# Kernel optimization log

Measured on AMD Instinct MI355X. Metric: run time of the kernel, lower is better.

## Reference

```python
import jax, jax.numpy as jnp
import numpy as np

B, L, C, D = 32, 4096, 64, 128
TOPK = max(1, int(L * 0.5))


def setup_inputs() -> dict:
    key = jax.random.key(0)
    ks = jax.random.split(key, 9)
    s = lambda k, sh: jax.random.normal(k, sh, dtype=jnp.float32) * 0.02
    return {
        "x": jax.random.normal(ks[0], (B, L, C), dtype=jnp.float32),
        "score_w": s(ks[1], (C,)),
        "score_b": jnp.zeros((), jnp.float32),
        "sparse_w": s(ks[2], (C, D)),
        "sparse_b": jnp.zeros((D,), jnp.float32),
        "full_w": s(ks[3], (C, D)),
        "full_b": jnp.zeros((D,), jnp.float32),
        "ln_g": jnp.ones((D,), jnp.float32),
        "ln_b": jnp.zeros((D,), jnp.float32),
    }


def _layernorm(h, g, b, eps=1e-5):
    mu = jnp.mean(h, axis=-1, keepdims=True)
    var = jnp.mean(jnp.square(h - mu), axis=-1, keepdims=True)
    return (h - mu) * jax.lax.rsqrt(var + eps) * g + b


def reference(x, score_w, score_b, sparse_w, sparse_b, full_w, full_b, ln_g, ln_b):
    # scores: (B, L)
    scores = jnp.einsum("blc,c->bl", x, score_w) + score_b
    _, idx = jax.lax.top_k(scores, TOPK)              # (B, K)
    sparse_x = jnp.take_along_axis(x, idx[:, :, None], axis=1)  # (B, K, C)
    sparse_feat = jax.nn.gelu(jnp.einsum("bkc,cd->bkd", sparse_x, sparse_w) + sparse_b, approximate=False)
    sparse_agg = jnp.mean(sparse_feat, axis=1, keepdims=True)   # (B, 1, D)
    full_feat = jnp.einsum("blc,cd->bld", x, full_w) + full_b   # (B, L, D)
    out = _layernorm(full_feat + sparse_agg, ln_g, ln_b)
    return out
```

## Files before the change

kernel.cpp:

```cpp
#include <hip/hip_runtime.h>
#include <math.h>

static constexpr int PB = 32;
static constexpr int PL = 4096;
static constexpr int PC = 64;
static constexpr int PD = 128;
static constexpr int PK = 2048;

typedef __attribute__((ext_vector_type(8))) short bf16x8;
typedef __attribute__((ext_vector_type(4))) float f32x4;

#define MFMA_BF16(A, B, C) __builtin_amdgcn_mfma_f32_16x16x32_bf16(A, B, C, 0, 0, 0)

__device__ inline short f2bf(float f) {
  unsigned u = __float_as_uint(f);
  u += 0x7FFFu + ((u >> 16) & 1u);
  return (short)(u >> 16);
}

__device__ inline unsigned f2key(float f) {
  unsigned u = __float_as_uint(f);
  return (u & 0x80000000u) ? ~u : (u | 0x80000000u);
}

__global__ __launch_bounds__(256) void scores_kernel(
    const float* __restrict__ x, const float* __restrict__ score_w,
    const float* __restrict__ score_b, const float* __restrict__ sparse_w,
    const float* __restrict__ full_w, float* __restrict__ scores,
    short* __restrict__ xbf, unsigned* __restrict__ wtfg,
    unsigned* __restrict__ ghist) {
  int tid = threadIdx.x;
  int blk = blockIdx.x;
  int b = blk >> 5;

  if (blk < 2) {
    const float* w = (blk == 0) ? sparse_w : full_w;
    unsigned* dst = wtfg + blk * 4096;
    for (int i = tid; i < 4096; i += 256) {
      int d = i & 127, cp = i >> 7, c = cp * 2;
      float va = w[(size_t)c * PD + d];
      float vb = w[(size_t)(c + 1) * PD + d];
      unsigned lo = (unsigned short)f2bf(va);
      unsigned hi = (unsigned short)f2bf(vb);
      int t = d >> 4, dl = d & 15, h = c >> 5, cq = (c >> 3) & 3, jp = (c & 7) >> 1;
      dst[(((t * 2 + h) * 4 + cq) * 16 + dl) * 4 + jp] = lo | (hi << 16);
    }
  }

  int r  = tid >> 4;
  int c4 = tid & 15;
  float4 wv = *(const float4*)(score_w + c4 * 4);
  float sb0 = score_b[0];
  unsigned* gh = ghist + (size_t)b * 2048;

  #pragma unroll
  for (int it = 0; it < 8; ++it) {
    int row = blk * 128 + it * 16 + r;
    float4 xv = *(const float4*)(x + (size_t)row * PC + c4 * 4);
    short4 xbv;
    xbv.x = f2bf(xv.x); xbv.y = f2bf(xv.y); xbv.z = f2bf(xv.z); xbv.w = f2bf(xv.w);
    *(short4*)(xbf + (size_t)row * PC + c4 * 4) = xbv;
    float v = xv.x * wv.x + xv.y * wv.y + xv.z * wv.z + xv.w * wv.w;
    #pragma unroll
    for (int off = 1; off < 16; off <<= 1) v += __shfl_xor(v, off);
    if (c4 == 0) {
      float sv = v + sb0;
      scores[row] = sv;
      atomicAdd(&gh[f2key(sv) >> 21], 1u);
    }
  }
}

template <int N>
__device__ inline void suffix_scan(const unsigned* cnt, int tid, int lane, int wid,
                                   unsigned* hbuf, unsigned* wsum) {
  unsigned tsum = 0;
  #pragma unroll
  for (int i = 0; i < N; ++i) tsum += cnt[i];
  unsigned v = tsum;
  #pragma unroll
  for (int off = 1; off < 64; off <<= 1) {
    unsigned t = __shfl_down(v, off);
    if (lane + off < 64) v += t;
  }
  if (lane == 0) wsum[wid] = v;
  __syncthreads();
  unsigned add = 0;
  #pragma unroll
  for (int w = 0; w < 4; ++w) if (w > wid) add += wsum[w];
  unsigned run = v + add - tsum;
  #pragma unroll
  for (int i = N - 1; i >= 0; --i) { run += cnt[i]; hbuf[tid * N + i] = run; }
  if (tid == 0) hbuf[256 * N] = 0;
  __syncthreads();
}

__global__ __launch_bounds__(256) void select_kernel(
    const float* __restrict__ scores, const unsigned* __restrict__ ghist,
    int* __restrict__ selidx, float* __restrict__ agg) {
  __shared__ unsigned hbuf[2049];
  __shared__ unsigned wsum[4];
  __shared__ unsigned sh_pfx, sh_need;

  int tid = threadIdx.x;
  int lane = tid & 63;
  int wid  = tid >> 6;
  int b = blockIdx.x;
  const float* sc = scores + (size_t)b * PL;

  unsigned k[16];
  #pragma unroll
  for (int q = 0; q < 4; ++q) {
    float4 f = *(const float4*)(sc + tid * 16 + q * 4);
    k[q * 4 + 0] = f2key(f.x);
    k[q * 4 + 1] = f2key(f.y);
    k[q * 4 + 2] = f2key(f.z);
    k[q * 4 + 3] = f2key(f.w);
  }
  if (tid == 0) sh_need = (unsigned)PK;
  if (tid < PD) agg[(size_t)b * PD + tid] = 0.f;

  {
    const unsigned* gh = ghist + (size_t)b * 2048;
    uint4 c0 = *(const uint4*)(gh + tid * 8);
    uint4 c1 = *(const uint4*)(gh + tid * 8 + 4);
    unsigned cnt[8] = {c0.x, c0.y, c0.z, c0.w, c1.x, c1.y, c1.z, c1.w};
    suffix_scan<8>(cnt, tid, lane, wid, hbuf, wsum);
    unsigned need = sh_need;
    #pragma unroll
    for (int i = 0; i < 8; ++i) {
      int kk = tid * 8 + i;
      if (hbuf[kk] >= need && hbuf[kk + 1] < need) {
        sh_pfx  = (unsigned)kk << 21;
        sh_need = need - hbuf[kk + 1];
      }
    }
  }

  {
    #pragma unroll
    for (int i = 0; i < 8; ++i) hbuf[tid * 8 + i] = 0u;
    __syncthreads();
    unsigned pfx = sh_pfx, need = sh_need;
    #pragma unroll
    for (int j = 0; j < 16; ++j) {
      if ((k[j] & 0xFFE00000u) == pfx)
        atomicAdd(&hbuf[(k[j] >> 10) & 2047u], 1u);
    }
    __syncthreads();
    unsigned cnt[8];
    #pragma unroll
    for (int i = 0; i < 8; ++i) cnt[i] = hbuf[tid * 8 + i];
    __syncthreads();
    suffix_scan<8>(cnt, tid, lane, wid, hbuf, wsum);
    #pragma unroll
    for (int i = 0; i < 8; ++i) {
      int kk = tid * 8 + i;
      if (hbuf[kk] >= need && hbuf[kk + 1] < need) {
        sh_pfx  = pfx | ((unsigned)kk << 10);
        sh_need = need - hbuf[kk + 1];
      }
    }
  }

  {
    #pragma unroll
    for (int i = 0; i < 4; ++i) hbuf[tid * 4 + i] = 0u;
    __syncthreads();
    unsigned pfx = sh_pfx, need = sh_need;
    #pragma unroll
    for (int j = 0; j < 16; ++j) {
      if ((k[j] & 0xFFFFFC00u) == pfx)
        atomicAdd(&hbuf[k[j] & 1023u], 1u);
    }
    __syncthreads();
    unsigned cnt[4];
    #pragma unroll
    for (int i = 0; i < 4; ++i) cnt[i] = hbuf[tid * 4 + i];
    __syncthreads();
    suffix_scan<4>(cnt, tid, lane, wid, hbuf, wsum);
    #pragma unroll
    for (int i = 0; i < 4; ++i) {
      int kk = tid * 4 + i;
      if (hbuf[kk] >= need && hbuf[kk + 1] < need) {
        sh_pfx  = pfx | (unsigned)kk;
        sh_need = need - hbuf[kk + 1];
      }
    }
  }
  __syncthreads();
  unsigned T = sh_pfx;
  unsigned needEq = sh_need;

  int base = tid * 16;
  unsigned ceq = 0;
  #pragma unroll
  for (int j = 0; j < 16; ++j) ceq += (k[j] == T);

  unsigned v1 = ceq;
  #pragma unroll
  for (int off = 1; off < 64; off <<= 1) {
    unsigned t = __shfl_up(v1, off);
    if (lane >= off) v1 += t;
  }
  if (lane == 63) wsum[wid] = v1;
  __syncthreads();
  unsigned add1 = 0;
  #pragma unroll
  for (int w = 0; w < 4; ++w) if (w < wid) add1 += wsum[w];
  unsigned eqbase = v1 + add1 - ceq;
  __syncthreads();

  unsigned csel = 0, eqr = eqbase;
  #pragma unroll
  for (int j = 0; j < 16; ++j) {
    if (k[j] > T) csel++;
    else if (k[j] == T) { if (eqr < needEq) csel++; eqr++; }
  }
  unsigned v2 = csel;
  #pragma unroll
  for (int off = 1; off < 64; off <<= 1) {
    unsigned t = __shfl_up(v2, off);
    if (lane >= off) v2 += t;
  }
  if (lane == 63) wsum[wid] = v2;
  __syncthreads();
  unsigned add2 = 0;
  #pragma unroll
  for (int w = 0; w < 4; ++w) if (w < wid) add2 += wsum[w];
  unsigned pos = v2 + add2 - csel;

  eqr = eqbase;
  int* outp = selidx + (size_t)b * PK;
  #pragma unroll
  for (int j = 0; j < 16; ++j) {
    bool sel;
    if (k[j] > T) sel = true;
    else if (k[j] == T) { sel = (eqr < needEq); eqr++; }
    else sel = false;
    if (sel) outp[pos++] = base + j;
  }
}

__device__ inline void stage_wtf(const unsigned* __restrict__ g, unsigned* lds, int tid) {
  #pragma unroll
  for (int q = 0; q < 4; ++q) {
    uint4 v = *(const uint4*)(g + q * 1024 + tid * 4);
    *(uint4*)(lds + q * 1024 + tid * 4) = v;
  }
}

__global__ __launch_bounds__(256, 3) void sparse_kernel(
    const short* __restrict__ xbf, const unsigned* __restrict__ wtfg,
    const float* __restrict__ sparse_b, const int* __restrict__ selidx,
    float* __restrict__ agg) {
  __shared__ unsigned WTf[4096];
  __shared__ float red[PD];
  int tid = threadIdx.x;
  stage_wtf(wtfg, WTf, tid);
  if (tid < PD) red[tid] = 0.f;
  __syncthreads();

  int lane = tid & 63, wid = tid >> 6;
  int ln = lane & 15, quad = lane >> 4;
  int b  = blockIdx.x >> 4;
  int rb = blockIdx.x & 15;
  int j0 = rb * 128 + wid * 32 + ln;
  const int* sel = selidx + (size_t)b * PK;
  int r0 = sel[j0], r1 = sel[j0 + 16];

  const short* xb = xbf + (size_t)b * PL * PC;
  const short* p0 = xb + (size_t)r0 * PC + quad * 8;
  const short* p1 = xb + (size_t)r1 * PC + quad * 8;
  bf16x8 a00 = *(const bf16x8*)p0, a01 = *(const bf16x8*)(p0 + 32);
  bf16x8 a10 = *(const bf16x8*)p1, a11 = *(const bf16x8*)(p1 + 32);

  f32x4 acc0[8], acc1[8];
  #pragma unroll
  for (int t = 0; t < 8; ++t) { acc0[t] = (f32x4){0.f,0.f,0.f,0.f}; acc1[t] = (f32x4){0.f,0.f,0.f,0.f}; }

  const short* wb = (const short*)WTf + lane * 8;
  #pragma unroll
  for (int t = 0; t < 8; ++t) {
    bf16x8 b0 = *(const bf16x8*)(wb + (2 * t) * 512);
    bf16x8 b1 = *(const bf16x8*)(wb + (2 * t + 1) * 512);
    acc0[t] = MFMA_BF16(a00, b0, acc0[t]);
    acc0[t] = MFMA_BF16(a01, b1, acc0[t]);
    acc1[t] = MFMA_BF16(a10, b0, acc1[t]);
    acc1[t] = MFMA_BF16(a11, b1, acc1[t]);
  }

  #pragma unroll
  for (int t = 0; t < 8; ++t) {
    float bias = sparse_b[t * 16 + ln];
    float s = 0.f;
    #pragma unroll
    for (int i = 0; i < 4; ++i) {
      float v0 = acc0[t][i] + bias;
      s += 0.5f * v0 * (1.0f + erff(v0 * 0.70710678118654752f));
      float v1 = acc1[t][i] + bias;
      s += 0.5f * v1 * (1.0f + erff(v1 * 0.70710678118654752f));
    }
    s += __shfl_xor(s, 16);
    s += __shfl_xor(s, 32);
    if (quad == 0) atomicAdd(&red[t * 16 + ln], s);
  }
  __syncthreads();
  if (tid < PD) atomicAdd(&agg[(size_t)b * PD + tid], red[tid]);
}

__global__ __launch_bounds__(256, 3) void full_ln_kernel(
    const short* __restrict__ xbf, const unsigned* __restrict__ wtfg,
    const float* __restrict__ full_b, const float* __restrict__ ln_g,
    const float* __restrict__ ln_b, const float* __restrict__ agg,
    float* __restrict__ out) {
  __shared__ unsigned WTf[4096];
  int tid = threadIdx.x;
  stage_wtf(wtfg, WTf, tid);
  __syncthreads();

  int lane = tid & 63, wid = tid >> 6;
  int ln = lane & 15, quad = lane >> 4;
  int rowbase = blockIdx.x * 128 + wid * 32;
  int b = rowbase >> 12;

  const float invK = 1.0f / (float)PK;
  float bias[8], gg[8], bb[8];
  #pragma unroll
  for (int t = 0; t < 8; ++t) {
    int d = t * 16 + ln;
    bias[t] = full_b[d] + agg[(size_t)b * PD + d] * invK;
    gg[t] = ln_g[d];
    bb[t] = ln_b[d];
  }

  const short* p0 = xbf + (size_t)(rowbase + ln) * PC + quad * 8;
  const short* p1 = xbf + (size_t)(rowbase + 16 + ln) * PC + quad * 8;
  bf16x8 a00 = *(const bf16x8*)p0, a01 = *(const bf16x8*)(p0 + 32);
  bf16x8 a10 = *(const bf16x8*)p1, a11 = *(const bf16x8*)(p1 + 32);

  f32x4 acc0[8], acc1[8];
  #pragma unroll
  for (int t = 0; t < 8; ++t) { acc0[t] = (f32x4){0.f,0.f,0.f,0.f}; acc1[t] = (f32x4){0.f,0.f,0.f,0.f}; }

  const short* wb = (const short*)WTf + lane * 8;
  #pragma unroll
  for (int t = 0; t < 8; ++t) {
    bf16x8 b0 = *(const bf16x8*)(wb + (2 * t) * 512);
    bf16x8 b1 = *(const bf16x8*)(wb + (2 * t + 1) * 512);
    acc0[t] = MFMA_BF16(a00, b0, acc0[t]);
    acc0[t] = MFMA_BF16(a01, b1, acc0[t]);
    acc1[t] = MFMA_BF16(a10, b0, acc1[t]);
    acc1[t] = MFMA_BF16(a11, b1, acc1[t]);
  }

#define LN_EPILOGUE(ACC, GOFF) do {                                          \
    float s_[4] = {0.f,0.f,0.f,0.f}, ss_[4] = {0.f,0.f,0.f,0.f};             \
    _Pragma("unroll")                                                        \
    for (int t = 0; t < 8; ++t) {                                            \
      _Pragma("unroll")                                                      \
      for (int i = 0; i < 4; ++i) {                                          \
        float h_ = ACC[t][i] + bias[t];                                      \
        ACC[t][i] = h_;                                                      \
        s_[i] += h_; ss_[i] += h_ * h_;                                      \
      }                                                                      \
    }                                                                        \
    _Pragma("unroll")                                                        \
    for (int i = 0; i < 4; ++i) {                                            \
      _Pragma("unroll")                                                      \
      for (int off = 1; off < 16; off <<= 1) {                               \
        s_[i]  += __shfl_xor(s_[i], off);                                    \
        ss_[i] += __shfl_xor(ss_[i], off);                                   \
      }                                                                      \
    }                                                                        \
    _Pragma("unroll")                                                        \
    for (int i = 0; i < 4; ++i) {                                            \
      float mu_  = s_[i] * (1.0f / 128.0f);                                  \
      float var_ = ss_[i] * (1.0f / 128.0f) - mu_ * mu_;                     \
      float inv_ = rsqrtf(var_ + 1e-5f);                                     \
      int r_ = rowbase + (GOFF) + quad * 4 + i;                              \
      float* op_ = out + (size_t)r_ * PD + ln;                               \
      _Pragma("unroll")                                                      \
      for (int t = 0; t < 8; ++t)                                            \
        op_[t * 16] = (ACC[t][i] - mu_) * inv_ * gg[t] + bb[t];              \
    }                                                                        \
  } while (0)

  LN_EPILOGUE(acc0, 0);
  LN_EPILOGUE(acc1, 16);
#undef LN_EPILOGUE
}

extern "C" void kernel_launch(void* const* d_in, const int* in_sizes, int n_in,
                              void* d_out, int out_size, void* d_ws, size_t ws_size,
                              hipStream_t stream) {
  const float* x        = (const float*)d_in[0];
  const float* score_w  = (const float*)d_in[1];
  const float* score_b  = (const float*)d_in[2];
  const float* sparse_w = (const float*)d_in[3];
  const float* sparse_b = (const float*)d_in[4];
  const float* full_w   = (const float*)d_in[5];
  const float* full_b   = (const float*)d_in[6];
  const float* ln_g     = (const float*)d_in[7];
  const float* ln_b     = (const float*)d_in[8];
  float* out = (float*)d_out;

  char* ws = (char*)d_ws;
  float*    scores = (float*)ws;
  int*      selidx = (int*)(ws + (512 << 10));
  float*    agg    = (float*)(ws + (768 << 10));
  unsigned* wtfg   = (unsigned*)(ws + (784 << 10));
  unsigned* ghist  = (unsigned*)(ws + (816 << 10));
  short*    xbf    = (short*)(ws + (1072 << 10));

  hipMemsetAsync(ghist, 0, (size_t)PB * 2048 * sizeof(unsigned), stream);
  scores_kernel<<<PB * PL / 128, 256, 0, stream>>>(x, score_w, score_b, sparse_w,
                                                   full_w, scores, xbf, wtfg, ghist);
  select_kernel<<<PB, 256, 0, stream>>>(scores, ghist, selidx, agg);
  sparse_kernel<<<PB * (PK / 128), 256, 0, stream>>>(xbf, wtfg, sparse_b, selidx, agg);
  full_ln_kernel<<<PB * PL / 128, 256, 0, stream>>>(xbf, wtfg + 4096, full_b,
                                                    ln_g, ln_b, agg, out);
}
```

Measured before the change: 146.1 us.

## Fuse top-k selection into sparse kernel and drop global histogram and memset

Removes the separate select kernel, the global histogram with its memset, and the global atomics in the scores kernel. Each sparse block now redoes the full radix top-k selection for its batch row on an LDS histogram and keeps only the 128 selected indices it needs in shared memory. agg zeroing moves into the scores kernel. This cuts two launches and a global round trip of indices, but repeats the selection work 16 times per batch and adds LDS use to the sparse kernel.

```diff
diff --git a/kernel.cpp b/kernel.cpp
--- a/kernel.cpp
+++ b/kernel.cpp
@@ -28,10 +28,9 @@
     const float* __restrict__ score_b, const float* __restrict__ sparse_w,
     const float* __restrict__ full_w, float* __restrict__ scores,
     short* __restrict__ xbf, unsigned* __restrict__ wtfg,
-    unsigned* __restrict__ ghist) {
+    float* __restrict__ agg) {
   int tid = threadIdx.x;
   int blk = blockIdx.x;
-  int b = blk >> 5;
 
   if (blk < 2) {
     const float* w = (blk == 0) ? sparse_w : full_w;
@@ -46,12 +45,13 @@
       dst[(((t * 2 + h) * 4 + cq) * 16 + dl) * 4 + jp] = lo | (hi << 16);
     }
   }
+  if ((blk & 31) == 0 && tid < PD)
+    agg[(size_t)(blk >> 5) * PD + tid] = 0.f;
 
   int r  = tid >> 4;
   int c4 = tid & 15;
   float4 wv = *(const float4*)(score_w + c4 * 4);
   float sb0 = score_b[0];
-  unsigned* gh = ghist + (size_t)b * 2048;
 
   #pragma unroll
   for (int it = 0; it < 8; ++it) {
@@ -63,11 +63,15 @@
     float v = xv.x * wv.x + xv.y * wv.y + xv.z * wv.z + xv.w * wv.w;
     #pragma unroll
     for (int off = 1; off < 16; off <<= 1) v += __shfl_xor(v, off);
-    if (c4 == 0) {
-      float sv = v + sb0;
-      scores[row] = sv;
-      atomicAdd(&gh[f2key(sv) >> 21], 1u);
-    }
+    if (c4 == 0) scores[row] = v + sb0;
+  }
+}
+
+__device__ inline void stage_wtf(const unsigned* __restrict__ g, unsigned* lds, int tid) {
+  #pragma unroll
+  for (int q = 0; q < 4; ++q) {
+    uint4 v = *(const uint4*)(g + q * 1024 + tid * 4);
+    *(uint4*)(lds + q * 1024 + tid * 4) = v;
   }
 }
 
@@ -95,17 +99,24 @@
   __syncthreads();
 }
 
-__global__ __launch_bounds__(256) void select_kernel(
-    const float* __restrict__ scores, const unsigned* __restrict__ ghist,
-    int* __restrict__ selidx, float* __restrict__ agg) {
+__global__ __launch_bounds__(256, 3) void sparse_kernel(
+    const short* __restrict__ xbf, const unsigned* __restrict__ wtfg,
+    const float* __restrict__ sparse_b, const float* __restrict__ scores,
+    float* __restrict__ agg) {
+  __shared__ unsigned WTf[4096];
+  __shared__ float red[PD];
   __shared__ unsigned hbuf[2049];
   __shared__ unsigned wsum[4];
   __shared__ unsigned sh_pfx, sh_need;
+  __shared__ int sel_l[128];
 
   int tid = threadIdx.x;
-  int lane = tid & 63;
-  int wid  = tid >> 6;
-  int b = blockIdx.x;
+  stage_wtf(wtfg, WTf, tid);
+  if (tid < PD) red[tid] = 0.f;
+
+  int lane = tid & 63, wid = tid >> 6;
+  int b  = blockIdx.x >> 4;
+  int rb = blockIdx.x & 15;
   const float* sc = scores + (size_t)b * PL;
 
   unsigned k[16];
@@ -118,15 +129,20 @@
     k[q * 4 + 3] = f2key(f.w);
   }
   if (tid == 0) sh_need = (unsigned)PK;
-  if (tid < PD) agg[(size_t)b * PD + tid] = 0.f;
 
   {
-    const unsigned* gh = ghist + (size_t)b * 2048;
-    uint4 c0 = *(const uint4*)(gh + tid * 8);
-    uint4 c1 = *(const uint4*)(gh + tid * 8 + 4);
-    unsigned cnt[8] = {c0.x, c0.y, c0.z, c0.w, c1.x, c1.y, c1.z, c1.w};
+    #pragma unroll
+    for (int i = 0; i < 8; ++i) hbuf[tid * 8 + i] = 0u;
+    __syncthreads();
+    unsigned need = sh_need;
+    #pragma unroll
+    for (int j = 0; j < 16; ++j) atomicAdd(&hbuf[k[j] >> 21], 1u);
+    __syncthreads();
+    unsigned cnt[8];
+    #pragma unroll
+    for (int i = 0; i < 8; ++i) cnt[i] = hbuf[tid * 8 + i];
+    __syncthreads();
     suffix_scan<8>(cnt, tid, lane, wid, hbuf, wsum);
-    unsigned need = sh_need;
     #pragma unroll
     for (int i = 0; i < 8; ++i) {
       int kk = tid * 8 + i;
@@ -230,44 +246,24 @@
   for (int w = 0; w < 4; ++w) if (w < wid) add2 += wsum[w];
   unsigned pos = v2 + add2 - csel;
 
+  int lo = rb * 128;
   eqr = eqbase;
-  int* outp = selidx + (size_t)b * PK;
   #pragma unroll
   for (int j = 0; j < 16; ++j) {
     bool sel;
     if (k[j] > T) sel = true;
     else if (k[j] == T) { sel = (eqr < needEq); eqr++; }
     else sel = false;
-    if (sel) outp[pos++] = base + j;
-  }
-}
-
-__device__ inline void stage_wtf(const unsigned* __restrict__ g, unsigned* lds, int tid) {
-  #pragma unroll
-  for (int q = 0; q < 4; ++q) {
-    uint4 v = *(const uint4*)(g + q * 1024 + tid * 4);
-    *(uint4*)(lds + q * 1024 + tid * 4) = v;
-  }
-}
-
-__global__ __launch_bounds__(256, 3) void sparse_kernel(
-    const short* __restrict__ xbf, const unsigned* __restrict__ wtfg,
-    const float* __restrict__ sparse_b, const int* __restrict__ selidx,
-    float* __restrict__ agg) {
-  __shared__ unsigned WTf[4096];
-  __shared__ float red[PD];
-  int tid = threadIdx.x;
-  stage_wtf(wtfg, WTf, tid);
-  if (tid < PD) red[tid] = 0.f;
-  __syncthreads();
-
-  int lane = tid & 63, wid = tid >> 6;
+    if (sel) {
+      int p = (int)pos++;
+      if (p >= lo && p < lo + 128) sel_l[p - lo] = base + j;
+    }
+  }
+  __syncthreads();
+
   int ln = lane & 15, quad = lane >> 4;
-  int b  = blockIdx.x >> 4;
-  int rb = blockIdx.x & 15;
-  int j0 = rb * 128 + wid * 32 + ln;
-  const int* sel = selidx + (size_t)b * PK;
-  int r0 = sel[j0], r1 = sel[j0 + 16];
+  int jl = wid * 32 + ln;
+  int r0 = sel_l[jl], r1 = sel_l[jl + 16];
 
   const short* xb = xbf + (size_t)b * PL * PC;
   const short* p0 = xb + (size_t)r0 * PC + quad * 8;
@@ -407,17 +403,13 @@
 
   char* ws = (char*)d_ws;
   float*    scores = (float*)ws;
-  int*      selidx = (int*)(ws + (512 << 10));
-  float*    agg    = (float*)(ws + (768 << 10));
-  unsigned* wtfg   = (unsigned*)(ws + (784 << 10));
-  unsigned* ghist  = (unsigned*)(ws + (816 << 10));
-  short*    xbf    = (short*)(ws + (1072 << 10));
-
-  hipMemsetAsync(ghist, 0, (size_t)PB * 2048 * sizeof(unsigned), stream);
+  float*    agg    = (float*)(ws + (512 << 10));
+  unsigned* wtfg   = (unsigned*)(ws + (528 << 10));
+  short*    xbf    = (short*)(ws + (560 << 10));
+
   scores_kernel<<<PB * PL / 128, 256, 0, stream>>>(x, score_w, score_b, sparse_w,
-                                                   full_w, scores, xbf, wtfg, ghist);
-  select_kernel<<<PB, 256, 0, stream>>>(scores, ghist, selidx, agg);
-  sparse_kernel<<<PB * (PK / 128), 256, 0, stream>>>(xbf, wtfg, sparse_b, selidx, agg);
+                                                   full_w, scores, xbf, wtfg, agg);
+  sparse_kernel<<<PB * (PK / 128), 256, 0, stream>>>(xbf, wtfg, sparse_b, scores, agg);
   full_ln_kernel<<<PB * PL / 128, 256, 0, stream>>>(xbf, wtfg + 4096, full_b,
                                                     ln_g, ln_b, agg, out);
 }
```

After: 132.5 us. 1.1x faster.
